# Kernel tuning notes

Measured on AMD Instinct MI355X. Metric: run time of the kernel, lower is better.

The kernel has to match this reference:

```python
import jax, jax.numpy as jnp
import numpy as np

N_NODES = 100000
N_EDGES = 1600000
F_IN, HIDDEN, N_CLASS = 256, 64, 2


def _gcn_conv(x, W, b, src, dst, norm, n):
    # PyG GCNConv: linear (no bias) -> normalized scatter-add -> bias
    h = x @ W                                  # [N, out]
    msg = h[src] * norm[:, None]               # gather + scale, [E+N, out]
    agg = jax.ops.segment_sum(msg, dst, num_segments=n)
    return agg + b


def setup_inputs() -> dict:
    key = jax.random.key(0)
    ks = jax.random.split(key, 8)
    x = jax.random.normal(ks[0], (N_NODES, F_IN), dtype=jnp.float32)
    edge_index = jax.random.randint(ks[1], (2, N_EDGES), 0, N_NODES, dtype=jnp.int32)
    W1 = jax.random.normal(ks[2], (F_IN, HIDDEN), dtype=jnp.float32) / np.sqrt(F_IN).astype(np.float32)
    b1 = jnp.zeros((HIDDEN,), dtype=jnp.float32)
    W2 = jax.random.normal(ks[3], (HIDDEN, HIDDEN), dtype=jnp.float32) / np.sqrt(HIDDEN).astype(np.float32)
    b2 = jnp.zeros((HIDDEN,), dtype=jnp.float32)
    W3 = jax.random.normal(ks[4], (HIDDEN, N_CLASS), dtype=jnp.float32) / np.sqrt(HIDDEN).astype(np.float32)
    b3 = jnp.zeros((N_CLASS,), dtype=jnp.float32)
    return {"x": x, "edge_index": edge_index, "W1": W1, "b1": b1, "W2": W2, "b2": b2, "W3": W3, "b3": b3}


def reference(x, edge_index, W1, b1, W2, b2, W3, b3):
    n = x.shape[0]
    # add self-loops (GCNConv default)
    loops = jnp.arange(n, dtype=edge_index.dtype)
    src = jnp.concatenate([edge_index[0], loops])
    dst = jnp.concatenate([edge_index[1], loops])
    # symmetric normalization D^-1/2 A_hat D^-1/2
    deg = jax.ops.segment_sum(jnp.ones_like(src, dtype=x.dtype), dst, num_segments=n)
    deg_inv_sqrt = jnp.where(deg > 0, jax.lax.rsqrt(jnp.maximum(deg, 1.0)), 0.0)
    norm = deg_inv_sqrt[src] * deg_inv_sqrt[dst]
    # layer 1 + relu (dropout is identity in eval mode)
    h = jax.nn.relu(_gcn_conv(x, W1, b1, src, dst, norm, n))
    # layer 2 + relu
    h = jax.nn.relu(_gcn_conv(h, W2, b2, src, dst, norm, n))
    # output layer + log_softmax
    h = _gcn_conv(h, W3, b3, src, dst, norm, n)
    return jax.nn.log_softmax(h, axis=1)
```

## Files before the change

kernel.cpp:

```cpp
#include <hip/hip_runtime.h>
#include <math.h>

#define F_IN 256
#define HID  64
#define BSH  8
#define BSPAN 256
#define CHUNK 16384
#define NBK_MAX 512

typedef __bf16   bf16x8 __attribute__((ext_vector_type(8)));
typedef float    floatx4 __attribute__((ext_vector_type(4)));
typedef _Float16 half8 __attribute__((ext_vector_type(8)));

__global__ __launch_bounds__(256) void k_hist(const int* __restrict__ dst,
                                              int* __restrict__ cntT,
                                              int E, int NCH, int NBK) {
    __shared__ int hist[NBK_MAX];
    int t = threadIdx.x, c = blockIdx.x;
    hist[t] = 0; hist[t + 256] = 0;
    __syncthreads();
    int base = c * CHUNK;
#pragma unroll 4
    for (int j = 0; j < CHUNK / 256; j++) {
        int e = base + j * 256 + t;
        if (e < E) atomicAdd(&hist[dst[e] >> BSH], 1);
    }
    __syncthreads();
    for (int b = t; b < NBK; b += 256) cntT[b * NCH + c] = hist[b];
}

__global__ __launch_bounds__(256) void k_scanA(const int* __restrict__ cntT,
                                               int* __restrict__ off,
                                               int* __restrict__ partials, int S) {
    __shared__ int sh[256];
    int tid = threadIdx.x;
    int base = blockIdx.x * 1024 + tid * 4;
    int v[4];
    int s = 0;
#pragma unroll
    for (int j = 0; j < 4; j++) {
        int idx = base + j;
        v[j] = (idx < S) ? cntT[idx] : 0;
        s += v[j];
    }
    sh[tid] = s;
    __syncthreads();
    int mysum = s;
    for (int o = 1; o < 256; o <<= 1) {
        int tv = (tid >= o) ? sh[tid - o] : 0;
        __syncthreads();
        sh[tid] += tv;
        __syncthreads();
    }
    int pref = sh[tid] - mysum;
#pragma unroll
    for (int j = 0; j < 4; j++) {
        int idx = base + j;
        if (idx < S) off[idx] = pref;
        pref += v[j];
    }
    if (tid == 255) partials[blockIdx.x] = sh[255];
}

__global__ void k_scanB(int* __restrict__ partials, int* __restrict__ off,
                        int nblk, int S) {
    if (blockIdx.x == 0 && threadIdx.x == 0) {
        int run = 0;
        for (int b = 0; b < nblk; b++) { int t = partials[b]; partials[b] = run; run += t; }
        off[S] = run;
    }
}

__global__ void k_scanC(int* __restrict__ off, const int* __restrict__ partials, int S) {
    int i = blockIdx.x * blockDim.x + threadIdx.x;
    if (i < S) off[i] += partials[i >> 10];
}

__global__ __launch_bounds__(256) void k_sortwrite(const int* __restrict__ src,
                                                   const int* __restrict__ dst,
                                                   const int* __restrict__ off,
                                                   int* __restrict__ ebuf,
                                                   int E, int NCH, int NBK) {
    __shared__ int cur[NBK_MAX];
    int t = threadIdx.x, c = blockIdx.x;
    for (int b = t; b < NBK; b += 256) cur[b] = off[b * NCH + c];
    __syncthreads();
    int base = c * CHUNK;
#pragma unroll 4
    for (int j = 0; j < CHUNK / 256; j++) {
        int e = base + j * 256 + t;
        if (e < E) {
            int s = src[e];
            int d = dst[e];
            int pos = atomicAdd(&cur[d >> BSH], 1);
            ebuf[pos] = (s << BSH) | (d & (BSPAN - 1));
        }
    }
}

__global__ __launch_bounds__(256) void k_bucket_csr(const int* __restrict__ off,
                                                    const int* __restrict__ ebuf,
                                                    int* __restrict__ rp,
                                                    float* __restrict__ dinv,
                                                    int* __restrict__ esrc,
                                                    int N, int NCH, int NBK) {
    __shared__ int cnt[BSPAN];
    __shared__ int sh[BSPAN];
    int b = blockIdx.x, t = threadIdx.x;
    int base = off[b * NCH];
    int end  = off[(b + 1) * NCH];

    cnt[t] = 0;
    __syncthreads();
    for (int i = base + t; i < end; i += 256) atomicAdd(&cnt[ebuf[i] & (BSPAN - 1)], 1);
    __syncthreads();

    int c = cnt[t];
    sh[t] = c;
    __syncthreads();
    for (int o = 1; o < 256; o <<= 1) {
        int tv = (t >= o) ? sh[t - o] : 0;
        __syncthreads();
        sh[t] += tv;
        __syncthreads();
    }
    int excl = sh[t] - c;

    int node = (b << BSH) + t;
    if (node < N) {
        rp[node] = base + excl;
        dinv[node] = rsqrtf((float)(1 + c));
    }
    if (b == NBK - 1 && t == 0) rp[N] = end;
    __syncthreads();

    cnt[t] = base + excl;
    __syncthreads();
    for (int i = base + t; i < end; i += 256) {
        int v = ebuf[i];
        int p = atomicAdd(&cnt[v & (BSPAN - 1)], 1);
        esrc[p] = v >> BSH;
    }
}

__global__ __launch_bounds__(256) void k_prepw(const float* __restrict__ W1,
                                               __bf16* __restrict__ f1h, __bf16* __restrict__ f1l,
                                               const float* __restrict__ W2,
                                               __bf16* __restrict__ f2h, __bf16* __restrict__ f2l) {
    int t = threadIdx.x + blockIdx.x * blockDim.x;
    for (int idx = t; idx < 16384; idx += 2048) {
        int j = idx & 7, lane = (idx >> 3) & 63, ch2 = (idx >> 9) & 7, c = idx >> 12;
        int k = ch2 * 32 + (lane >> 4) * 8 + j, col = c * 16 + (lane & 15);
        float w = W1[k * 64 + col];
        __bf16 h = (__bf16)w;
        f1h[idx] = h; f1l[idx] = (__bf16)(w - (float)h);
    }
    for (int idx = t; idx < 4096; idx += 2048) {
        int j = idx & 7, lane = (idx >> 3) & 63, ch2 = (idx >> 9) & 1, c = idx >> 10;
        int k = ch2 * 32 + (lane >> 4) * 8 + j, col = c * 16 + (lane & 15);
        float w = W2[k * 64 + col];
        __bf16 h = (__bf16)w;
        f2h[idx] = h; f2l[idx] = (__bf16)(w - (float)h);
    }
}

__global__ __launch_bounds__(256) void k_gemm1(const float* __restrict__ A,
                                               const __bf16* __restrict__ BfH,
                                               const __bf16* __restrict__ BfL,
                                               const float* __restrict__ dinv,
                                               _Float16* __restrict__ C, int nrows) {
    constexpr int K = 256, KC = 64, NCHK = 4, NCH32 = 8;
    __shared__ float As[2][64 * KC];

    const int t = threadIdx.x;
    const int wave = t >> 6, lane = t & 63;
    const int m = lane & 15, q = lane >> 4;
    const int row0 = blockIdx.x * 64;

    const int s_sub = lane >> 4;
    const int s_seg = lane & 15;

    auto stage = [&](int ch, int buf) {
#pragma unroll
        for (int j = 0; j < 4; j++) {
            int lr = wave * 16 + j * 4 + s_sub;
            int gr = row0 + lr; if (gr > nrows - 1) gr = nrows - 1;
            int gs = (s_seg - lr) & 15;
            const float* g = A + (size_t)gr * K + ch * KC + gs * 4;
            float* l = &As[buf][(size_t)lr * KC + s_seg * 4];
            __builtin_amdgcn_global_load_lds(
                (const __attribute__((address_space(1))) void*)g,
                (__attribute__((address_space(3))) void*)l, 16, 0, 0);
        }
    };

    floatx4 acc[4] = {{0.f, 0.f, 0.f, 0.f}, {0.f, 0.f, 0.f, 0.f},
                      {0.f, 0.f, 0.f, 0.f}, {0.f, 0.f, 0.f, 0.f}};

    stage(0, 0);
    __syncthreads();

    for (int ch = 0; ch < NCHK; ch++) {
        if (ch + 1 < NCHK) stage(ch + 1, (ch + 1) & 1);

        const float* arow = &As[ch & 1][(size_t)(wave * 16 + m) * KC];
#pragma unroll
        for (int jj = 0; jj < 2; jj++) {
            int ch2 = ch * 2 + jj;
            int s0 = jj * 8 + q * 2;
            float4 v0 = *(const float4*)(arow + (((s0 + m) & 15) * 4));
            float4 v1 = *(const float4*)(arow + (((s0 + 1 + m) & 15) * 4));
            float af[8] = {v0.x, v0.y, v0.z, v0.w, v1.x, v1.y, v1.z, v1.w};
            bf16x8 ah, al;
#pragma unroll
            for (int j = 0; j < 8; j++) {
                __bf16 h = (__bf16)af[j];
                ah[j] = h;
                al[j] = (__bf16)(af[j] - (float)h);
            }
#pragma unroll
            for (int c = 0; c < 4; c++) {
                const bf16x8 bh = *(const bf16x8*)(BfH + ((size_t)(c * NCH32 + ch2) * 64 + lane) * 8);
                const bf16x8 bl = *(const bf16x8*)(BfL + ((size_t)(c * NCH32 + ch2) * 64 + lane) * 8);
                acc[c] = __builtin_amdgcn_mfma_f32_16x16x32_bf16(ah, bh, acc[c], 0, 0, 0);
                acc[c] = __builtin_amdgcn_mfma_f32_16x16x32_bf16(al, bh, acc[c], 0, 0, 0);
                acc[c] = __builtin_amdgcn_mfma_f32_16x16x32_bf16(ah, bl, acc[c], 0, 0, 0);
            }
        }
        __syncthreads();
    }

#pragma unroll
    for (int i = 0; i < 4; i++) {
        int r = row0 + wave * 16 + q * 4 + i;
        if (r < nrows) {
            float di = dinv[r];
#pragma unroll
            for (int c = 0; c < 4; c++)
                C[(size_t)r * 64 + c * 16 + m] = (_Float16)(acc[c][i] * di);
        }
    }
}

__global__ __launch_bounds__(256) void k_gemm2(const _Float16* __restrict__ A,
                                               const __bf16* __restrict__ BfH,
                                               const __bf16* __restrict__ BfL,
                                               const float* __restrict__ dinv,
                                               _Float16* __restrict__ C, int nrows) {
    __shared__ _Float16 As[64 * 64];
    const int t = threadIdx.x;
    const int wave = t >> 6, lane = t & 63;
    const int m = lane & 15, q = lane >> 4;
    const int row0 = blockIdx.x * 64;

#pragma unroll
    for (int j = 0; j < 2; j++) {
        int lr = j * 32 + wave * 8 + (lane >> 3);
        int p  = lane & 7;
        int gr = row0 + lr; if (gr > nrows - 1) gr = nrows - 1;
        int gs = (p - lr) & 7;
        const _Float16* g = A + (size_t)gr * 64 + gs * 8;
        _Float16* l = &As[(size_t)lr * 64 + p * 8];
        __builtin_amdgcn_global_load_lds(
            (const __attribute__((address_space(1))) void*)g,
            (__attribute__((address_space(3))) void*)l, 16, 0, 0);
    }
    __syncthreads();

    floatx4 acc[4] = {{0.f, 0.f, 0.f, 0.f}, {0.f, 0.f, 0.f, 0.f},
                      {0.f, 0.f, 0.f, 0.f}, {0.f, 0.f, 0.f, 0.f}};

    const _Float16* arow = &As[(size_t)(wave * 16 + m) * 64];
#pragma unroll
    for (int jj = 0; jj < 2; jj++) {
        int s0 = jj * 4 + q;
        half8 v = *(const half8*)(arow + (((s0 + m) & 7) * 8));
        bf16x8 ah, al;
#pragma unroll
        for (int j = 0; j < 8; j++) {
            float f = (float)v[j];
            __bf16 h = (__bf16)f;
            ah[j] = h;
            al[j] = (__bf16)(f - (float)h);
        }
#pragma unroll
        for (int c = 0; c < 4; c++) {
            const bf16x8 bh = *(const bf16x8*)(BfH + ((size_t)(c * 2 + jj) * 64 + lane) * 8);
            const bf16x8 bl = *(const bf16x8*)(BfL + ((size_t)(c * 2 + jj) * 64 + lane) * 8);
            acc[c] = __builtin_amdgcn_mfma_f32_16x16x32_bf16(ah, bh, acc[c], 0, 0, 0);
            acc[c] = __builtin_amdgcn_mfma_f32_16x16x32_bf16(al, bh, acc[c], 0, 0, 0);
            acc[c] = __builtin_amdgcn_mfma_f32_16x16x32_bf16(ah, bl, acc[c], 0, 0, 0);
        }
    }

#pragma unroll
    for (int i = 0; i < 4; i++) {
        int r = row0 + wave * 16 + q * 4 + i;
        if (r < nrows) {
            float di = dinv[r];
#pragma unroll
            for (int c = 0; c < 4; c++)
                C[(size_t)r * 64 + c * 16 + m] = (_Float16)(acc[c][i] * di);
        }
    }
}

template <int MODE>
__global__ __launch_bounds__(256) void k_agg64(const _Float16* __restrict__ hs,
                                               const float* __restrict__ dinv,
                                               const int* __restrict__ rp,
                                               const int* __restrict__ esrc,
                                               const float* __restrict__ bias,
                                               const float* __restrict__ W3,
                                               void* __restrict__ out, int n) {
    int lane = threadIdx.x & 63;
    int nid = blockIdx.x * 4 + (threadIdx.x >> 6);
    if (nid >= n) return;
    nid = __builtin_amdgcn_readfirstlane(nid);

    float dii = dinv[nid];
    int e0 = rp[nid];
    int e1 = rp[nid + 1];

    float a0 = (float)hs[(size_t)nid * 64 + lane];
    float a1 = 0.f, a2 = 0.f, a3 = 0.f, a4 = 0.f, a5 = 0.f, a6 = 0.f, a7 = 0.f;

    for (int e = e0; e < e1; e += 8) {
        int last = e1 - 1;
        int i0 = esrc[e];
        int i1 = esrc[min(e + 1, last)];
        int i2 = esrc[min(e + 2, last)];
        int i3 = esrc[min(e + 3, last)];
        int i4 = esrc[min(e + 4, last)];
        int i5 = esrc[min(e + 5, last)];
        int i6 = esrc[min(e + 6, last)];
        int i7 = esrc[min(e + 7, last)];
        float v0 = (float)hs[(size_t)i0 * 64 + lane];
        float v1 = (float)hs[(size_t)i1 * 64 + lane];
        float v2 = (float)hs[(size_t)i2 * 64 + lane];
        float v3 = (float)hs[(size_t)i3 * 64 + lane];
        float v4 = (float)hs[(size_t)i4 * 64 + lane];
        float v5 = (float)hs[(size_t)i5 * 64 + lane];
        float v6 = (float)hs[(size_t)i6 * 64 + lane];
        float v7 = (float)hs[(size_t)i7 * 64 + lane];
        a0 += v0;
        a1 += (e + 1 <= last) ? v1 : 0.f;
        a2 += (e + 2 <= last) ? v2 : 0.f;
        a3 += (e + 3 <= last) ? v3 : 0.f;
        a4 += (e + 4 <= last) ? v4 : 0.f;
        a5 += (e + 5 <= last) ? v5 : 0.f;
        a6 += (e + 6 <= last) ? v6 : 0.f;
        a7 += (e + 7 <= last) ? v7 : 0.f;
    }

    float acc = ((a0 + a1) + (a2 + a3)) + ((a4 + a5) + (a6 + a7));
    acc = acc * dii + bias[lane];
    acc = fmaxf(acc, 0.f);

    if (MODE == 0) {
        ((_Float16*)out)[(size_t)nid * 64 + lane] = (_Float16)acc;
    } else {
        float2 w3 = ((const float2*)W3)[lane];
        float p0 = acc * w3.x;
        float p1 = acc * w3.y;
#pragma unroll
        for (int o = 32; o > 0; o >>= 1) {
            p0 += __shfl_xor(p0, o, 64);
            p1 += __shfl_xor(p1, o, 64);
        }
        if (lane == 0) ((float2*)out)[nid] = make_float2(p0 * dii, p1 * dii);
    }
}

__global__ __launch_bounds__(256) void k_final(const float2* __restrict__ h3s,
                                               const float* __restrict__ dinv,
                                               const int* __restrict__ rp,
                                               const int* __restrict__ esrc,
                                               const float* __restrict__ b3,
                                               float* __restrict__ out, int n) {
    int i = blockIdx.x * blockDim.x + threadIdx.x;
    if (i >= n) return;
    float dii = dinv[i];
    float2 h = h3s[i];
    float ax = h.x, ay = h.y;
    float bx = 0.f, by = 0.f, cx = 0.f, cy = 0.f, dx = 0.f, dy = 0.f;
    int e0 = rp[i], e1 = rp[i + 1];
    for (int e = e0; e < e1; e += 4) {
        int last = e1 - 1;
        int s0 = esrc[e];
        int s1 = esrc[min(e + 1, last)];
        int s2 = esrc[min(e + 2, last)];
        int s3 = esrc[min(e + 3, last)];
        float2 v0 = h3s[s0];
        float2 v1 = h3s[s1];
        float2 v2 = h3s[s2];
        float2 v3 = h3s[s3];
        ax += v0.x; ay += v0.y;
        bx += (e + 1 <= last) ? v1.x : 0.f; by += (e + 1 <= last) ? v1.y : 0.f;
        cx += (e + 2 <= last) ? v2.x : 0.f; cy += (e + 2 <= last) ? v2.y : 0.f;
        dx += (e + 3 <= last) ? v3.x : 0.f; dy += (e + 3 <= last) ? v3.y : 0.f;
    }
    float l0 = ((ax + bx) + (cx + dx)) * dii + b3[0];
    float l1 = ((ay + by) + (cy + dy)) * dii + b3[1];
    float m = fmaxf(l0, l1);
    float lse = m + logf(expf(l0 - m) + expf(l1 - m));
    ((float2*)out)[i] = make_float2(l0 - lse, l1 - lse);
}

extern "C" void kernel_launch(void* const* d_in, const int* in_sizes, int n_in,
                              void* d_out, int out_size, void* d_ws, size_t ws_size,
                              hipStream_t stream) {
    const float* x   = (const float*)d_in[0];
    const int*   ei  = (const int*)d_in[1];
    const float* W1  = (const float*)d_in[2];
    const float* b1  = (const float*)d_in[3];
    const float* W2  = (const float*)d_in[4];
    const float* b2  = (const float*)d_in[5];
    const float* W3  = (const float*)d_in[6];
    const float* b3  = (const float*)d_in[7];
    float* out = (float*)d_out;

    const int N = in_sizes[0] / F_IN;
    const int E = in_sizes[1] / 2;
    const int* src = ei;
    const int* dst = ei + E;

    const int NBK = (N + BSPAN - 1) / BSPAN;
    const int NCH = (E + CHUNK - 1) / CHUNK;
    const int S   = NBK * NCH;

    char* p = (char*)d_ws;
    auto alloc = [&](size_t bytes) -> void* {
        void* r = (void*)p;
        p += (bytes + 255) & ~(size_t)255;
        return r;
    };
    int*      cntT     = (int*)alloc((size_t)S * 4);
    int*      off      = (int*)alloc((size_t)(S + 1) * 4);
    int*      partials = (int*)alloc(4096);
    int*      ebuf     = (int*)alloc((size_t)E * 4);
    int*      esrc     = (int*)alloc((size_t)E * 4);
    int*      rp       = (int*)alloc((size_t)(N + 1) * 4);
    float*    dinv     = (float*)alloc((size_t)N * 4);
    _Float16* bufA     = (_Float16*)alloc((size_t)N * HID * 2);
    _Float16* bufB     = (_Float16*)alloc((size_t)N * HID * 2);
    float*    h3       = (float*)alloc((size_t)N * 2 * 4);
    __bf16*   f1h      = (__bf16*)alloc(16384 * 2);
    __bf16*   f1l      = (__bf16*)alloc(16384 * 2);
    __bf16*   f2h      = (__bf16*)alloc(4096 * 2);
    __bf16*   f2l      = (__bf16*)alloc(4096 * 2);

    const int T = 256;
    int scanBlocks = (S + 1023) / 1024;

    k_prepw<<<8, T, 0, stream>>>(W1, f1h, f1l, W2, f2h, f2l);

    k_hist<<<NCH, T, 0, stream>>>(dst, cntT, E, NCH, NBK);
    k_scanA<<<scanBlocks, T, 0, stream>>>(cntT, off, partials, S);
    k_scanB<<<1, 64, 0, stream>>>(partials, off, scanBlocks, S);
    k_scanC<<<(S + T - 1) / T, T, 0, stream>>>(off, partials, S);
    k_sortwrite<<<NCH, T, 0, stream>>>(src, dst, off, ebuf, E, NCH, NBK);
    k_bucket_csr<<<NBK, T, 0, stream>>>(off, ebuf, rp, dinv, esrc, N, NCH, NBK);

    int gemmBlocks = (N + 63) / 64;
    k_gemm1<<<gemmBlocks, T, 0, stream>>>(x, f1h, f1l, dinv, bufA, N);
    k_agg64<0><<<(N + 3) / 4, T, 0, stream>>>(bufA, dinv, rp, esrc, b1, nullptr, bufB, N);

    k_gemm2<<<gemmBlocks, T, 0, stream>>>(bufB, f2h, f2l, dinv, bufA, N);
    k_agg64<1><<<(N + 3) / 4, T, 0, stream>>>(bufA, dinv, rp, esrc, b2, W3, h3, N);

    k_final<<<(N + T - 1) / T, T, 0, stream>>>((const float2*)h3, dinv, rp, esrc, b3, out, N);
}
```

Measured before the change: 404.6 us.

## Vectorize GCN aggregation gathers: 4 edges per wave with half4 loads, cross-quarter reduce

The 64-wide aggregation kernel now splits each wave into four 16-lane groups. Each group gathers a different edge's row with 8-byte half4 loads, instead of the whole wave reading one fp16 per lane per edge. Partial sums are combined across the groups with shuffles, and the output projection reduction is adjusted to match. The histogram CHUNK is reduced, giving more blocks, and log-softmax uses a cheaper two-class formula based on log1p. Wider loads and more edges in flight should make better use of memory bandwidth in the irregular gather, at the cost of extra shuffles and some lanes idling on the tail of short neighbor lists.

```diff
diff --git a/kernel.cpp b/kernel.cpp
--- a/kernel.cpp
+++ b/kernel.cpp
@@ -5,12 +5,13 @@
 #define HID  64
 #define BSH  8
 #define BSPAN 256
-#define CHUNK 16384
+#define CHUNK 4096
 #define NBK_MAX 512
 
 typedef __bf16   bf16x8 __attribute__((ext_vector_type(8)));
 typedef float    floatx4 __attribute__((ext_vector_type(4)));
 typedef _Float16 half8 __attribute__((ext_vector_type(8)));
+typedef _Float16 half4v __attribute__((ext_vector_type(4)));
 
 __global__ __launch_bounds__(256) void k_hist(const int* __restrict__ dst,
                                               int* __restrict__ cntT,
@@ -314,6 +315,8 @@
                                                const float* __restrict__ W3,
                                                void* __restrict__ out, int n) {
     int lane = threadIdx.x & 63;
+    int qe = lane >> 4;
+    int fg = lane & 15;
     int nid = blockIdx.x * 4 + (threadIdx.x >> 6);
     if (nid >= n) return;
     nid = __builtin_amdgcn_readfirstlane(nid);
@@ -321,50 +324,56 @@
     float dii = dinv[nid];
     int e0 = rp[nid];
     int e1 = rp[nid + 1];
-
-    float a0 = (float)hs[(size_t)nid * 64 + lane];
-    float a1 = 0.f, a2 = 0.f, a3 = 0.f, a4 = 0.f, a5 = 0.f, a6 = 0.f, a7 = 0.f;
-
-    for (int e = e0; e < e1; e += 8) {
-        int last = e1 - 1;
-        int i0 = esrc[e];
-        int i1 = esrc[min(e + 1, last)];
-        int i2 = esrc[min(e + 2, last)];
-        int i3 = esrc[min(e + 3, last)];
-        int i4 = esrc[min(e + 4, last)];
-        int i5 = esrc[min(e + 5, last)];
-        int i6 = esrc[min(e + 6, last)];
-        int i7 = esrc[min(e + 7, last)];
-        float v0 = (float)hs[(size_t)i0 * 64 + lane];
-        float v1 = (float)hs[(size_t)i1 * 64 + lane];
-        float v2 = (float)hs[(size_t)i2 * 64 + lane];
-        float v3 = (float)hs[(size_t)i3 * 64 + lane];
-        float v4 = (float)hs[(size_t)i4 * 64 + lane];
-        float v5 = (float)hs[(size_t)i5 * 64 + lane];
-        float v6 = (float)hs[(size_t)i6 * 64 + lane];
-        float v7 = (float)hs[(size_t)i7 * 64 + lane];
-        a0 += v0;
-        a1 += (e + 1 <= last) ? v1 : 0.f;
-        a2 += (e + 2 <= last) ? v2 : 0.f;
-        a3 += (e + 3 <= last) ? v3 : 0.f;
-        a4 += (e + 4 <= last) ? v4 : 0.f;
-        a5 += (e + 5 <= last) ? v5 : 0.f;
-        a6 += (e + 6 <= last) ? v6 : 0.f;
-        a7 += (e + 7 <= last) ? v7 : 0.f;
-    }
-
-    float acc = ((a0 + a1) + (a2 + a3)) + ((a4 + a5) + (a6 + a7));
-    acc = acc * dii + bias[lane];
-    acc = fmaxf(acc, 0.f);
+    int last = e1 - 1;
+
+    float a0 = 0.f, a1 = 0.f, a2 = 0.f, a3 = 0.f;
+    if (qe == 0) {
+        half4v sv = *(const half4v*)(hs + (size_t)nid * 64 + fg * 4);
+        a0 = (float)sv[0]; a1 = (float)sv[1]; a2 = (float)sv[2]; a3 = (float)sv[3];
+    }
+
+    for (int e = e0; e <= last; e += 16) {
+#pragma unroll
+        for (int u = 0; u < 4; u++) {
+            int slot = e + u * 4 + qe;
+            int idx = esrc[min(slot, last)];
+            half4v v = *(const half4v*)(hs + (size_t)idx * 64 + fg * 4);
+            if (slot <= last) {
+                a0 += (float)v[0]; a1 += (float)v[1];
+                a2 += (float)v[2]; a3 += (float)v[3];
+            }
+        }
+    }
+
+#pragma unroll
+    for (int o = 16; o <= 32; o <<= 1) {
+        a0 += __shfl_xor(a0, o, 64);
+        a1 += __shfl_xor(a1, o, 64);
+        a2 += __shfl_xor(a2, o, 64);
+        a3 += __shfl_xor(a3, o, 64);
+    }
+
+    float4 b4 = ((const float4*)bias)[fg];
+    a0 = fmaxf(a0 * dii + b4.x, 0.f);
+    a1 = fmaxf(a1 * dii + b4.y, 0.f);
+    a2 = fmaxf(a2 * dii + b4.z, 0.f);
+    a3 = fmaxf(a3 * dii + b4.w, 0.f);
 
     if (MODE == 0) {
-        ((_Float16*)out)[(size_t)nid * 64 + lane] = (_Float16)acc;
+        if (qe == 0) {
+            half4v o4;
+            o4[0] = (_Float16)a0; o4[1] = (_Float16)a1;
+            o4[2] = (_Float16)a2; o4[3] = (_Float16)a3;
+            *(half4v*)((_Float16*)out + (size_t)nid * 64 + fg * 4) = o4;
+        }
     } else {
-        float2 w3 = ((const float2*)W3)[lane];
-        float p0 = acc * w3.x;
-        float p1 = acc * w3.y;
-#pragma unroll
-        for (int o = 32; o > 0; o >>= 1) {
+        const float2* w3 = (const float2*)W3;
+        float2 w0 = w3[fg * 4 + 0], w1 = w3[fg * 4 + 1];
+        float2 w2 = w3[fg * 4 + 2], w3v = w3[fg * 4 + 3];
+        float p0 = a0 * w0.x + a1 * w1.x + a2 * w2.x + a3 * w3v.x;
+        float p1 = a0 * w0.y + a1 * w1.y + a2 * w2.y + a3 * w3v.y;
+#pragma unroll
+        for (int o = 1; o <= 8; o <<= 1) {
             p0 += __shfl_xor(p0, o, 64);
             p1 += __shfl_xor(p1, o, 64);
         }
@@ -402,8 +411,8 @@
     }
     float l0 = ((ax + bx) + (cx + dx)) * dii + b3[0];
     float l1 = ((ay + by) + (cy + dy)) * dii + b3[1];
-    float m = fmaxf(l0, l1);
-    float lse = m + logf(expf(l0 - m) + expf(l1 - m));
+    float mx = fmaxf(l0, l1);
+    float lse = mx + log1pf(__expf(-fabsf(l0 - l1)));
     ((float2*)out)[i] = make_float2(l0 - lse, l1 - lse);
 }
 
```

New measurement: 407.2 us. Within noise of the previous version (+0.6%).
